# Kernel optimization log

Hardware: AMD Instinct MI355X
Metric: run time of the kernel (lower is better)

The kernel has to match this reference:

```python
import jax, jax.numpy as jnp
import numpy as np

N = 100_000          # nodes
E = 3_200_000        # edges (avg degree 32)
NEG_SLOPE = 0.2      # PyG GATConv default


def _gat_conv(x, src, dst, W, a_src, a_dst, b, n):
    """Single-head PyG-style GATConv. src/dst already include self-loops."""
    h = x @ W                                   # [N, F_out]
    logits = (h @ a_src)[src] + (h @ a_dst)[dst]  # [E']
    e = jax.nn.leaky_relu(logits, NEG_SLOPE)
    m = jax.ops.segment_max(e, dst, num_segments=n)
    ex = jnp.exp(e - m[dst])                    # stable ragged softmax over in-edges
    s = jax.ops.segment_sum(ex, dst, num_segments=n)
    alpha = ex / (s[dst] + 1e-16)
    out = jax.ops.segment_sum(h[src] * alpha[:, None], dst, num_segments=n)
    return out + b


def setup_inputs() -> dict:
    key = jax.random.key(0)
    ks = jax.random.split(key, 20)
    x = jax.random.normal(ks[0], (N, 3), dtype=jnp.float32)
    edge_index = jax.random.randint(ks[1], (2, E), 0, N, dtype=jnp.int64)

    def lin(k, fin, fout):
        return jax.random.normal(k, (fin, fout), dtype=jnp.float32) * (1.0 / np.sqrt(fin))

    def att(k, f):
        return jax.random.normal(k, (f,), dtype=jnp.float32) * (1.0 / np.sqrt(f))

    inp = {"x": x, "edge_index": edge_index}
    # forward-direction convs
    inp["W1"], inp["as1"], inp["ad1"], inp["b1"] = lin(ks[2], 3, 16), att(ks[3], 16), att(ks[4], 16), jnp.zeros((16,), jnp.float32)
    inp["W2"], inp["as2"], inp["ad2"], inp["b2"] = lin(ks[5], 16, 1), att(ks[6], 1), att(ks[7], 1), jnp.zeros((1,), jnp.float32)
    # reverse-direction convs
    inp["W1r"], inp["as1r"], inp["ad1r"], inp["b1r"] = lin(ks[8], 3, 16), att(ks[9], 16), att(ks[10], 16), jnp.zeros((16,), jnp.float32)
    inp["W2r"], inp["as2r"], inp["ad2r"], inp["b2r"] = lin(ks[11], 16, 1), att(ks[12], 1), att(ks[13], 1), jnp.zeros((1,), jnp.float32)
    return inp


def reference(x, edge_index, W1, as1, ad1, b1, W2, as2, ad2, b2,
              W1r, as1r, ad1r, b1r, W2r, as2r, ad2r, b2r):
    n = x.shape[0]
    loops = jnp.arange(n, dtype=edge_index.dtype)
    # forward direction (self-loops appended, as PyG add_self_loops=True)
    src = jnp.concatenate([edge_index[0], loops])
    dst = jnp.concatenate([edge_index[1], loops])
    # reverse direction: stack([ei[1], ei[0]]) then self-loops
    rsrc = jnp.concatenate([edge_index[1], loops])
    rdst = jnp.concatenate([edge_index[0], loops])

    xf = jax.nn.relu(_gat_conv(x, src, dst, W1, as1, ad1, b1, n))
    xf = _gat_conv(xf, src, dst, W2, as2, ad2, b2, n)

    xr = jax.nn.relu(_gat_conv(x, rsrc, rdst, W1r, as1r, ad1r, b1r, n))
    xr = _gat_conv(xr, rsrc, rdst, W2r, as2r, ad2r, b2r, n)

    return (xf + xr) * 0.5
```

## Files before the change

### kernel.cpp

```cpp
#include <hip/hip_runtime.h>
#include <math.h>

#define NSLOPE 0.2f
#define BSH 8
#define BNODES 256
#define NID_MASK 0x1FFFF
#define SENT 0xFFFFFFFFu
#define CAP 10240
#define GB 256
#define RE 4096
#define MAXNS 1024
#define CPT (CAP / 512)

__device__ __forceinline__ float lrelu(float v) { return v > 0.f ? v : NSLOPE * v; }

__global__ void k_flag(const unsigned long long* __restrict__ p, int* __restrict__ flag) {
    int t = threadIdx.x;
    bool bad = false;
#pragma unroll
    for (int i = 0; i < 4; i++)
        if (p[t * 4 + i] >= (1ull << 32)) bad = true;
    unsigned long long mask = __ballot(bad);
    if (t == 0) *flag = (mask == 0ull) ? 1 : 0;
}

__global__ void k_prep(const float* __restrict__ x,
                       const float* __restrict__ as1, const float* __restrict__ ad1,
                       const float* __restrict__ as1r, const float* __restrict__ ad1r,
                       const float* __restrict__ W1, const float* __restrict__ W1r,
                       float4* __restrict__ rec4f, float4* __restrict__ rec4r,
                       float* __restrict__ s1df, float* __restrict__ s1dr,
                       int* __restrict__ gcur, int NS, int N) {
    int i = blockIdx.x * blockDim.x + threadIdx.x;
    if (i < NS) gcur[i] = 0;
    if (i >= N) return;
    float x0 = x[3 * i], x1 = x[3 * i + 1], x2 = x[3 * i + 2];
    float ssf = 0.f, sdf = 0.f, ssr = 0.f, sdr = 0.f;
#pragma unroll
    for (int k = 0; k < 16; k++) {
        float hf = x0 * W1[k] + x1 * W1[16 + k] + x2 * W1[32 + k];
        ssf += hf * as1[k];
        sdf += hf * ad1[k];
        float hr = x0 * W1r[k] + x1 * W1r[16 + k] + x2 * W1r[32 + k];
        ssr += hr * as1r[k];
        sdr += hr * ad1r[k];
    }
    rec4f[i] = make_float4(x0, x1, x2, ssf);
    rec4r[i] = make_float4(x0, x1, x2, ssr);
    s1df[i] = sdf; s1dr[i] = sdr;
}

__global__ void __launch_bounds__(512) k_scatsort(
        const void* __restrict__ ei, long long E, const int* __restrict__ flag,
        int NB, int NS, int* __restrict__ gcur, unsigned* __restrict__ bin) {
    __shared__ unsigned stg[2 * RE];
    __shared__ unsigned short stgs[2 * RE];
    __shared__ int cnt[MAXNS];
    __shared__ int bs[MAXNS + 1];
    __shared__ int gpos[MAXNS];
    int t = threadIdx.x;
    int fl = *flag;
    long long chunk = (E + GB - 1) / GB;
    long long cstart = (long long)blockIdx.x * chunk;
    long long cend = cstart + chunk; if (cend > E) cend = E;

    for (long long rs = cstart; rs < cend; rs += RE) {
        int ne = (int)min((long long)RE, cend - rs);
        unsigned recs[16]; unsigned short ss[16];
        int nrec = 0;
#pragma unroll
        for (int k = 0; k < 8; k++) {
            int idx = t + k * 512;
            if (idx < ne) {
                long long i = rs + idx;
                int u, v;
                if (fl) {
                    const long long* p = (const long long*)ei;
                    u = (int)p[i]; v = (int)p[E + i];
                } else {
                    const int* p = (const int*)ei;
                    u = p[i]; v = p[E + i];
                }
                recs[nrec] = (unsigned)u | ((unsigned)(v & (BNODES - 1)) << 17);
                ss[nrec++] = (unsigned short)(v >> BSH);
                recs[nrec] = (unsigned)v | ((unsigned)(u & (BNODES - 1)) << 17);
                ss[nrec++] = (unsigned short)(NB + (u >> BSH));
            }
        }
        for (int c = t; c < NS; c += 512) cnt[c] = 0;
        __syncthreads();
        for (int k = 0; k < nrec; k++) atomicAdd(&cnt[ss[k]], 1);
        __syncthreads();
        if (t < 64) {
            int vals[16]; int s = 0;
#pragma unroll
            for (int j = 0; j < 16; j++) {
                int idx = t * 16 + j;
                int vv = (idx < NS) ? cnt[idx] : 0;
                vals[j] = s; s += vv;
            }
            int incl = s;
#pragma unroll
            for (int od = 1; od < 64; od <<= 1) {
                int up = __shfl_up(incl, od);
                if (t >= od) incl += up;
            }
            int excl = incl - s;
#pragma unroll
            for (int j = 0; j < 16; j++) {
                int idx = t * 16 + j;
                if (idx < NS) { bs[idx] = excl + vals[j]; cnt[idx] = excl + vals[j]; }
            }
            if (t == 63) bs[NS] = incl;
        }
        __syncthreads();
        for (int k = 0; k < nrec; k++) {
            int p = atomicAdd(&cnt[ss[k]], 1);
            stg[p] = recs[k];
            stgs[p] = ss[k];
        }
        __syncthreads();
        for (int c = t; c < NS; c += 512) {
            int n = bs[c + 1] - bs[c];
            gpos[c] = n ? atomicAdd(&gcur[c], n) : 0;
        }
        __syncthreads();
        int total = bs[NS];
        for (int i = t; i < total; i += 512) {
            int s = stgs[i];
            int off = gpos[s] + (i - bs[s]);
            if (off < CAP) bin[(long long)s * CAP + off] = stg[i];
        }
        __syncthreads();
    }
}

__global__ void __launch_bounds__(512) k_bagg1(
        unsigned* __restrict__ bin, const int* __restrict__ gcur,
        const float4* __restrict__ rec4f, const float* __restrict__ s1df,
        const float4* __restrict__ rec4r, const float* __restrict__ s1dr,
        const float* __restrict__ b1, const float* __restrict__ W1,
        const float* __restrict__ W2,
        const float* __restrict__ as2, const float* __restrict__ ad2,
        const float* __restrict__ b1r, const float* __restrict__ W1r,
        const float* __restrict__ W2r,
        const float* __restrict__ as2r, const float* __restrict__ ad2r,
        float2* __restrict__ p2f, float* __restrict__ s2df,
        float2* __restrict__ p2r, float* __restrict__ s2dr,
        int* __restrict__ aoff, int* __restrict__ aend, int NB, int N) {
    int bb = blockIdx.x, dir = blockIdx.y;
    const float4* rec4 = dir ? rec4r : rec4f;
    const float* s1d = dir ? s1dr : s1df;
    const float* b1_ = dir ? b1r : b1;
    const float* W1_ = dir ? W1r : W1;
    const float* W2_ = dir ? W2r : W2;
    float as2v = dir ? as2r[0] : as2[0];
    float ad2v = dir ? ad2r[0] : ad2[0];
    float2* p2 = dir ? p2r : p2f;
    float* s2d = dir ? s2dr : s2df;

    int c = dir * NB + bb;
    long long base = (long long)c * CAP;
    int n = gcur[c]; if (n > CAP) n = CAP;
    int v0 = bb << BSH;
    int nv = N - v0; if (nv > BNODES) nv = BNODES;

    __shared__ int cnt[BNODES];
    __shared__ int loff[BNODES];
    __shared__ unsigned lds_u[CAP];
    int t = threadIdx.x;

    unsigned recs[CPT];
#pragma unroll
    for (int k = 0; k < CPT; k++) {
        int i = t + k * 512;
        recs[k] = (i < n) ? __builtin_nontemporal_load(bin + base + i) : SENT;
    }
    if (t < BNODES) cnt[t] = 0;
    __syncthreads();
#pragma unroll
    for (int k = 0; k < CPT; k++)
        if (recs[k] != SENT) atomicAdd(&cnt[recs[k] >> 17], 1);
    __syncthreads();
    if (t < BNODES) loff[t] = cnt[t];
    __syncthreads();
    for (int od = 1; od < BNODES; od <<= 1) {
        int tmp = (t < BNODES && t >= od) ? loff[t - od] : 0;
        __syncthreads();
        if (t < BNODES) loff[t] += tmp;
        __syncthreads();
    }
    if (t < BNODES) {
        int ex = loff[t] - cnt[t];
        loff[t] = ex;
        cnt[t] = ex;
    }
    __syncthreads();
#pragma unroll
    for (int k = 0; k < CPT; k++)
        if (recs[k] != SENT) {
            int p = atomicAdd(&cnt[recs[k] >> 17], 1);
            lds_u[p] = recs[k] & NID_MASK;
        }
    __syncthreads();
    int node = t >> 1, lane = t & 1;
    float sdv = (node < nv) ? s1d[v0 + node] : 0.f;
    float d = 0.f, a0 = 0.f, a1 = 0.f, a2 = 0.f;
    if (node < nv) {
        int ls = loff[node], le = cnt[node];
        for (int pos = ls + lane; pos < le; pos += 2) {
            unsigned u = lds_u[pos];
            float4 r = rec4[u];
            float w = __expf(lrelu(r.w + sdv));
            d += w; a0 += w * r.x; a1 += w * r.y; a2 += w * r.z;
        }
    }
    d  += __shfl_xor(d, 1);
    a0 += __shfl_xor(a0, 1);
    a1 += __shfl_xor(a1, 1);
    a2 += __shfl_xor(a2, 1);
    if (lane == 0 && node < nv) {
        int v = v0 + node;
        float4 r = rec4[v];
        float w = __expf(lrelu(r.w + sdv));
        float dd = d + w;
        float inv = 1.f / (dd + 1e-16f);
        float m0 = (a0 + w * r.x) * inv;
        float m1 = (a1 + w * r.y) * inv;
        float m2 = (a2 + w * r.z) * inv;
        float h2v = 0.f;
#pragma unroll
        for (int k = 0; k < 16; k++) {
            float o = m0 * W1_[k] + m1 * W1_[16 + k] + m2 * W1_[32 + k] + b1_[k];
            o = fmaxf(o, 0.f);
            h2v += o * W2_[k];
        }
        p2[v] = make_float2(h2v, h2v * as2v);
        s2d[v] = h2v * ad2v;
    }
    for (int i = t; i < n; i += 512) bin[base + i] = lds_u[i];
    if (t < nv) {
        aoff[dir * N + v0 + t] = (int)(base + loff[t]);
        aend[dir * N + v0 + t] = (int)(base + cnt[t]);
    }
}

__global__ void k_agg2(const unsigned* __restrict__ bin,
                       const int* __restrict__ aoff, const int* __restrict__ aend,
                       const float2* __restrict__ p2f, const float* __restrict__ s2df,
                       const float2* __restrict__ p2r, const float* __restrict__ s2dr,
                       const float* __restrict__ b2, const float* __restrict__ b2r,
                       float* __restrict__ out, int N) {
    int tid = blockIdx.x * blockDim.x + threadIdx.x;
    int v = tid >> 3;
    int lane = tid & 7;
    if (v >= N) return;
    float res[2];
#pragma unroll
    for (int dir = 0; dir < 2; dir++) {
        const float2* p2 = dir ? p2r : p2f;
        const float* s2d = dir ? s2dr : s2df;
        float bias = dir ? b2r[0] : b2[0];
        float sd = s2d[v];
        int st = aoff[dir * N + v], en = aend[dir * N + v];
        float d = 0.f, a = 0.f;
        if (lane == 0) {
            float2 ts = p2[v];
            float w = __expf(lrelu(ts.y + sd));
            d = w; a = w * ts.x;
        }
        int j = st + lane;
        for (; j + 24 < en; j += 32) {
            unsigned u0 = __builtin_nontemporal_load(bin + j);
            unsigned u1 = __builtin_nontemporal_load(bin + j + 8);
            unsigned u2 = __builtin_nontemporal_load(bin + j + 16);
            unsigned u3 = __builtin_nontemporal_load(bin + j + 24);
            float2 t0 = p2[u0];
            float2 t1 = p2[u1];
            float2 t2 = p2[u2];
            float2 t3 = p2[u3];
            float w0 = __expf(lrelu(t0.y + sd));
            float w1 = __expf(lrelu(t1.y + sd));
            float w2 = __expf(lrelu(t2.y + sd));
            float w3 = __expf(lrelu(t3.y + sd));
            d += (w0 + w1) + (w2 + w3);
            a += w0 * t0.x + w1 * t1.x + w2 * t2.x + w3 * t3.x;
        }
        for (; j < en; j += 8) {
            unsigned u = __builtin_nontemporal_load(bin + j);
            float2 t = p2[u];
            float w = __expf(lrelu(t.y + sd));
            d += w;
            a += w * t.x;
        }
#pragma unroll
        for (int mask = 1; mask < 8; mask <<= 1) {
            d += __shfl_xor(d, mask);
            a += __shfl_xor(a, mask);
        }
        res[dir] = a / (d + 1e-16f) + bias;
    }
    if (lane == 0) out[v] = 0.5f * (res[0] + res[1]);
}

extern "C" void kernel_launch(void* const* d_in, const int* in_sizes, int n_in,
                              void* d_out, int out_size, void* d_ws, size_t ws_size,
                              hipStream_t stream) {
    const float* x   = (const float*)d_in[0];
    const void*  ei  = d_in[1];
    const float* W1  = (const float*)d_in[2];
    const float* as1 = (const float*)d_in[3];
    const float* ad1 = (const float*)d_in[4];
    const float* b1  = (const float*)d_in[5];
    const float* W2  = (const float*)d_in[6];
    const float* as2 = (const float*)d_in[7];
    const float* ad2 = (const float*)d_in[8];
    const float* b2  = (const float*)d_in[9];
    const float* W1r  = (const float*)d_in[10];
    const float* as1r = (const float*)d_in[11];
    const float* ad1r = (const float*)d_in[12];
    const float* b1r  = (const float*)d_in[13];
    const float* W2r  = (const float*)d_in[14];
    const float* as2r = (const float*)d_in[15];
    const float* ad2r = (const float*)d_in[16];
    const float* b2r  = (const float*)d_in[17];

    const int N = in_sizes[0] / 3;
    const long long E = in_sizes[1] / 2;
    const int NB = (N + BNODES - 1) >> BSH;
    const int NS = 2 * NB;

    char* w = (char*)d_ws;
    size_t o = 0;
    auto A = [&](size_t bytes) { o = (o + 255) & ~(size_t)255; size_t r = o; o += bytes; return r; };
    size_t oFlag = A(64);
    size_t oR4f  = A(sizeof(float4) * N);
    size_t oR4r  = A(sizeof(float4) * N);
    size_t oS1df = A(sizeof(float) * N);
    size_t oS1dr = A(sizeof(float) * N);
    size_t oP2f  = A(sizeof(float2) * N);
    size_t oS2df = A(sizeof(float) * N);
    size_t oP2r  = A(sizeof(float2) * N);
    size_t oS2dr = A(sizeof(float) * N);
    size_t oAoff = A(sizeof(int) * 2 * N);
    size_t oAend = A(sizeof(int) * 2 * N);
    size_t oGcur = A(sizeof(int) * NS);
    size_t oBin  = A(sizeof(unsigned) * (size_t)NS * CAP);
    (void)ws_size; (void)n_in; (void)out_size;

    int*    flag = (int*)(w + oFlag);
    float4* rec4f = (float4*)(w + oR4f);
    float4* rec4r = (float4*)(w + oR4r);
    float*  s1df = (float*)(w + oS1df);
    float*  s1dr = (float*)(w + oS1dr);
    float2* p2f  = (float2*)(w + oP2f);
    float*  s2df = (float*)(w + oS2df);
    float2* p2r  = (float2*)(w + oP2r);
    float*  s2dr = (float*)(w + oS2dr);
    int*    aoff = (int*)(w + oAoff);
    int*    aend = (int*)(w + oAend);
    int*    gcur = (int*)(w + oGcur);
    unsigned* bin = (unsigned*)(w + oBin);

    dim3 gN((N + 255) / 256);
    dim3 gAgg1(NB, 2);
    dim3 gAgg2((N * 8 + 255) / 256);

    k_flag<<<1, 64, 0, stream>>>((const unsigned long long*)ei, flag);
    k_prep<<<gN, 256, 0, stream>>>(x, as1, ad1, as1r, ad1r, W1, W1r,
                                   rec4f, rec4r, s1df, s1dr, gcur, NS, N);
    k_scatsort<<<GB, 512, 0, stream>>>(ei, E, flag, NB, NS, gcur, bin);
    k_bagg1<<<gAgg1, 512, 0, stream>>>(bin, gcur, rec4f, s1df, rec4r, s1dr,
                                       b1, W1, W2, as2, ad2,
                                       b1r, W1r, W2r, as2r, ad2r,
                                       p2f, s2df, p2r, s2dr, aoff, aend, NB, N);
    k_agg2<<<gAgg2, 256, 0, stream>>>(bin, aoff, aend, p2f, s2df, p2r, s2dr,
                                      b2, b2r, (float*)d_out, N);
}
```

Measured before the change: 263.4 us.

## Replace count-scan-scatter staging with fixed per-bucket shared slots and spill list

The edge binning kernel no longer runs a two-pass count, prefix scan and scatter through a shared staging buffer. Each record instead claims a slot with an atomic in a fixed 12-entry shared slot per bucket, and overflow goes to a small spill list. Each thread then copies one bucket's slots to global bins. Grid size and chunk size also change, to 512 blocks of 2048 edges. This removes a scan and several barriers, but the global writes become per-thread serial loops that are poorly coalesced, and records are silently dropped if more than 256 overflow in one chunk.

After: 257.6 us. -2.2%, faster.

```diff
diff --git a/kernel.cpp b/kernel.cpp
--- a/kernel.cpp
+++ b/kernel.cpp
@@ -7,9 +7,10 @@
 #define NID_MASK 0x1FFFF
 #define SENT 0xFFFFFFFFu
 #define CAP 10240
-#define GB 256
-#define RE 4096
-#define MAXNS 1024
+#define GB 512
+#define RE 2048
+#define SLOT 12
+#define SPILLCAP 256
 #define CPT (CAP / 512)
 
 __device__ __forceinline__ float lrelu(float v) { return v > 0.f ? v : NSLOPE * v; }
@@ -53,11 +54,15 @@
 __global__ void __launch_bounds__(512) k_scatsort(
         const void* __restrict__ ei, long long E, const int* __restrict__ flag,
         int NB, int NS, int* __restrict__ gcur, unsigned* __restrict__ bin) {
-    __shared__ unsigned stg[2 * RE];
-    __shared__ unsigned short stgs[2 * RE];
-    __shared__ int cnt[MAXNS];
-    __shared__ int bs[MAXNS + 1];
-    __shared__ int gpos[MAXNS];
+    extern __shared__ unsigned smem[];
+    unsigned* slots = smem;
+    int* cnt  = (int*)(slots + (size_t)NS * SLOT);
+    int* gpos = cnt + NS;
+    int* spill_s = gpos + NS;
+    int* spill_p = spill_s + SPILLCAP;
+    unsigned* spill_r = (unsigned*)(spill_p + SPILLCAP);
+    int* spn = (int*)(spill_r + SPILLCAP);
+
     int t = threadIdx.x;
     int fl = *flag;
     long long chunk = (E + GB - 1) / GB;
@@ -66,70 +71,49 @@
 
     for (long long rs = cstart; rs < cend; rs += RE) {
         int ne = (int)min((long long)RE, cend - rs);
-        unsigned recs[16]; unsigned short ss[16];
-        int nrec = 0;
-#pragma unroll
-        for (int k = 0; k < 8; k++) {
+        for (int c = t; c < NS; c += 512) cnt[c] = 0;
+        if (t == 0) *spn = 0;
+        __syncthreads();
+#pragma unroll
+        for (int k = 0; k < RE / 512; k++) {
             int idx = t + k * 512;
             if (idx < ne) {
                 long long i = rs + idx;
                 int u, v;
-                if (fl) {
-                    const long long* p = (const long long*)ei;
-                    u = (int)p[i]; v = (int)p[E + i];
-                } else {
-                    const int* p = (const int*)ei;
-                    u = p[i]; v = p[E + i];
-                }
-                recs[nrec] = (unsigned)u | ((unsigned)(v & (BNODES - 1)) << 17);
-                ss[nrec++] = (unsigned short)(v >> BSH);
-                recs[nrec] = (unsigned)v | ((unsigned)(u & (BNODES - 1)) << 17);
-                ss[nrec++] = (unsigned short)(NB + (u >> BSH));
+                if (fl) { const long long* p = (const long long*)ei; u = (int)p[i]; v = (int)p[E + i]; }
+                else    { const int* p = (const int*)ei; u = p[i]; v = p[E + i]; }
+                unsigned r0 = (unsigned)u | ((unsigned)(v & (BNODES - 1)) << 17);
+                int s0 = v >> BSH;
+                unsigned r1 = (unsigned)v | ((unsigned)(u & (BNODES - 1)) << 17);
+                int s1 = NB + (u >> BSH);
+                int p0 = atomicAdd(&cnt[s0], 1);
+                if (p0 < SLOT) slots[s0 * SLOT + p0] = r0;
+                else { int sp = atomicAdd(spn, 1); if (sp < SPILLCAP) { spill_s[sp] = s0; spill_p[sp] = p0; spill_r[sp] = r0; } }
+                int p1 = atomicAdd(&cnt[s1], 1);
+                if (p1 < SLOT) slots[s1 * SLOT + p1] = r1;
+                else { int sp = atomicAdd(spn, 1); if (sp < SPILLCAP) { spill_s[sp] = s1; spill_p[sp] = p1; spill_r[sp] = r1; } }
             }
         }
-        for (int c = t; c < NS; c += 512) cnt[c] = 0;
-        __syncthreads();
-        for (int k = 0; k < nrec; k++) atomicAdd(&cnt[ss[k]], 1);
-        __syncthreads();
-        if (t < 64) {
-            int vals[16]; int s = 0;
-#pragma unroll
-            for (int j = 0; j < 16; j++) {
-                int idx = t * 16 + j;
-                int vv = (idx < NS) ? cnt[idx] : 0;
-                vals[j] = s; s += vv;
+        __syncthreads();
+        for (int c = t; c < NS; c += 512) {
+            int n = cnt[c];
+            gpos[c] = n ? atomicAdd(&gcur[c], n) : 0;
+        }
+        __syncthreads();
+        for (int c = t; c < NS; c += 512) {
+            int n = cnt[c]; if (n > SLOT) n = SLOT;
+            int g = gpos[c];
+            long long b = (long long)c * CAP;
+            for (int j = 0; j < n; j++) {
+                int off = g + j;
+                if (off < CAP) bin[b + off] = slots[c * SLOT + j];
             }
-            int incl = s;
-#pragma unroll
-            for (int od = 1; od < 64; od <<= 1) {
-                int up = __shfl_up(incl, od);
-                if (t >= od) incl += up;
-            }
-            int excl = incl - s;
-#pragma unroll
-            for (int j = 0; j < 16; j++) {
-                int idx = t * 16 + j;
-                if (idx < NS) { bs[idx] = excl + vals[j]; cnt[idx] = excl + vals[j]; }
-            }
-            if (t == 63) bs[NS] = incl;
-        }
-        __syncthreads();
-        for (int k = 0; k < nrec; k++) {
-            int p = atomicAdd(&cnt[ss[k]], 1);
-            stg[p] = recs[k];
-            stgs[p] = ss[k];
-        }
-        __syncthreads();
-        for (int c = t; c < NS; c += 512) {
-            int n = bs[c + 1] - bs[c];
-            gpos[c] = n ? atomicAdd(&gcur[c], n) : 0;
-        }
-        __syncthreads();
-        int total = bs[NS];
-        for (int i = t; i < total; i += 512) {
-            int s = stgs[i];
-            int off = gpos[s] + (i - bs[s]);
-            if (off < CAP) bin[(long long)s * CAP + off] = stg[i];
+        }
+        int nsp = *spn; if (nsp > SPILLCAP) nsp = SPILLCAP;
+        for (int i = t; i < nsp; i += 512) {
+            int s = spill_s[i];
+            int off = gpos[s] + spill_p[i];
+            if (off < CAP) bin[(long long)s * CAP + off] = spill_r[i];
         }
         __syncthreads();
     }
@@ -366,10 +350,16 @@
     dim3 gAgg1(NB, 2);
     dim3 gAgg2((N * 8 + 255) / 256);
 
+    size_t smem = sizeof(unsigned) * (size_t)NS * SLOT
+                + sizeof(int) * (size_t)NS * 2
+                + sizeof(int) * SPILLCAP * 2
+                + sizeof(unsigned) * SPILLCAP
+                + 64;
+
     k_flag<<<1, 64, 0, stream>>>((const unsigned long long*)ei, flag);
     k_prep<<<gN, 256, 0, stream>>>(x, as1, ad1, as1r, ad1r, W1, W1r,
                                    rec4f, rec4r, s1df, s1dr, gcur, NS, N);
-    k_scatsort<<<GB, 512, 0, stream>>>(ei, E, flag, NB, NS, gcur, bin);
+    k_scatsort<<<GB, 512, smem, stream>>>(ei, E, flag, NB, NS, gcur, bin);
     k_bagg1<<<gAgg1, 512, 0, stream>>>(bin, gcur, rec4f, s1df, rec4r, s1dr,
                                        b1, W1, W2, as2, ad2,
                                        b1r, W1r, W2r, as2r, ad2r,
```
